# Kernel tuning notes

Measured on AMD Instinct MI355X. Metric: run time of the kernel, lower is better.

The kernel has to match this reference:

```python
import jax, jax.numpy as jnp
import numpy as np

G = 128          # number of point-cloud groups
DOWNSAMPLE = 256 # points per group
D = 256          # feature dim


def _pairwise_dist(x, y):
    # x: [G, n, d], y: [G, m, d] -> Euclidean distances [G, n, m]
    x2 = jnp.sum(x * x, axis=-1)[:, :, None]
    y2 = jnp.sum(y * y, axis=-1)[:, None, :]
    d2 = jnp.maximum(x2 + y2 - 2.0 * jnp.einsum('gnd,gmd->gnm', x, y), 0.0)
    # safe sqrt (zero diagonal has zero distance, avoid NaN grads)
    return jnp.where(d2 > 0, jnp.sqrt(jnp.where(d2 > 0, d2, 1.0)), 0.0)


def setup_inputs() -> dict:
    key = jax.random.key(0)
    k1, k2 = jax.random.split(key)
    inp = jax.random.normal(k1, (G * DOWNSAMPLE, D), dtype=jnp.float32)
    tgt = jax.random.normal(k2, (G * DOWNSAMPLE, D), dtype=jnp.float32)
    return {"input": inp, "target": tgt, "downsample": DOWNSAMPLE}


def reference(input, target, downsample):
    # MMDLoss.forward: reshape to (-1, downsample, D), batched energy distance, mean
    x = input.reshape(-1, downsample, input.shape[-1])   # [G, n, D]
    y = target.reshape(-1, downsample, target.shape[-1]) # [G, m, D]
    # Energy distance (geomloss 'energy' kernel k(x,y) = -||x-y||, uniform weights):
    # L = mean_ij ||x_i - y_j|| - 0.5 mean_ij ||x_i - x_j|| - 0.5 mean_ij ||y_i - y_j||
    d_xy = jnp.mean(_pairwise_dist(x, y), axis=(1, 2))  # [G]
    d_xx = jnp.mean(_pairwise_dist(x, x), axis=(1, 2))  # [G]
    d_yy = jnp.mean(_pairwise_dist(y, y), axis=(1, 2))  # [G]
    loss_per_group = d_xy - 0.5 * d_xx - 0.5 * d_yy
    return jnp.mean(loss_per_group)
```

## Files before the change

kernel.cpp:

```cpp
#include <hip/hip_runtime.h>
#include <hip/hip_bf16.h>
#include <stdint.h>
#include <string.h>

typedef __attribute__((ext_vector_type(8))) short short8;
typedef __attribute__((ext_vector_type(4))) float floatx4;
typedef unsigned short u16;

#define NPTS 256
#define DIM  256
#define TILE 128
#define BKN  64
#define NITN (DIM / BKN)

static __device__ __forceinline__ uint32_t cvtsq2(float a, float b, float& s) {
    __hip_bfloat162 h = __float22bfloat162_rn(float2{a, b});
    uint32_t d;
    memcpy(&d, &h, 4);
    const float lo = __builtin_bit_cast(float, d << 16);
    const float hi = __builtin_bit_cast(float, d & 0xFFFF0000u);
    s += lo * lo + hi * hi;
    return d;
}
static __device__ __forceinline__ uint4 cvt8(const float4 u, const float4 v, float& s) {
    uint4 r;
    r.x = cvtsq2(u.x, u.y, s); r.y = cvtsq2(u.z, u.w, s);
    r.z = cvtsq2(v.x, v.w == v.w ? v.w : v.w, s), r.z = cvtsq2(v.x, v.y, s); r.w = cvtsq2(v.z, v.w, s);
    return r;
}

__global__ __launch_bounds__(256)
void mmd_prep(const float* __restrict__ X, const float* __restrict__ Y,
              u16* __restrict__ Zb, float* __restrict__ nrm,
              int totalRows, int halfRows) {
    const int gid = blockIdx.x * 256 + threadIdx.x;
    const int row = gid >> 5;
    if (row >= totalRows) return;
    const int sub = gid & 31;
    const float* src = (row < halfRows ? X + (size_t)row * DIM
                                       : Y + (size_t)(row - halfRows) * DIM) + sub * 8;
    const float4 a = *(const float4*)src;
    const float4 b = *(const float4*)(src + 4);
    float s = 0.0f;
    uint4 p;
    p.x = cvtsq2(a.x, a.y, s); p.y = cvtsq2(a.z, a.w, s);
    p.z = cvtsq2(b.x, b.y, s); p.w = cvtsq2(b.z, b.w, s);
    *(uint4*)(Zb + (size_t)row * DIM + sub * 8) = p;
    s += __shfl_xor(s, 1); s += __shfl_xor(s, 2); s += __shfl_xor(s, 4);
    s += __shfl_xor(s, 8); s += __shfl_xor(s, 16);
    if (sub == 0) nrm[row] = s;
}

static __device__ __forceinline__ void stage_tile(
    const u16* __restrict__ Zrow0,
    u16* ldsbase,
    int k0, int wv, int lane) {
    #pragma unroll
    for (int j = 0; j < 4; ++j) {
        const int cid = (wv * 4 + j) * 64 + lane;
        const int row = cid >> 3;
        const int cs  = cid & 7;
        const int cg  = cs ^ (row & 7);
        const u16* src = Zrow0 + (size_t)row * DIM + k0 + cg * 8;
        u16* dst = ldsbase + (size_t)(wv * 4 + j) * 512;
        __builtin_amdgcn_global_load_lds(
            (const __attribute__((address_space(1))) uint32_t*)src,
            (__attribute__((address_space(3))) uint32_t*)dst, 16, 0, 0);
    }
}

__global__ __launch_bounds__(256, 2)
void mmd_main(const u16* __restrict__ Zb, const float* __restrict__ nrm,
              float* __restrict__ out, float scale, int G) {
    int g, t;
    const int f = blockIdx.x;
    if ((G & 7) == 0) { const int xcd = f & 7, j = f >> 3; g = (j / 10) * 8 + xcd; t = j % 10; }
    else              { g = f / 10; t = f % 10; }

    int ptype, ti, tj; float w;
    if (t < 4)      { ptype = 0; ti = t >> 1; tj = t & 1; w = 1.0f; }
    else if (t < 7) { int u = t - 4; ptype = 1; ti = (u == 2); tj = (u >= 1); w = (u == 1) ? -1.0f : -0.5f; }
    else            { int u = t - 7; ptype = 2; ti = (u == 2); tj = (u >= 1); w = (u == 1) ? -1.0f : -0.5f; }

    const int half = G * NPTS;
    const int pbase = (ptype == 2) ? half : 0;
    const int qbase = (ptype == 1) ? 0 : half;
    const size_t prow0 = (size_t)pbase + (size_t)g * NPTS + (size_t)ti * TILE;
    const size_t qrow0 = (size_t)qbase + (size_t)g * NPTS + (size_t)tj * TILE;
    const bool symdiag = (ptype != 0) && (ti == tj);

    const u16* ZP = Zb + prow0 * DIM;
    const u16* ZQ = Zb + qrow0 * DIM;

    __shared__ __align__(16) u16 As[2][TILE * BKN];
    __shared__ __align__(16) u16 Bs[2][TILE * BKN];
    __shared__ float rnormS[TILE];
    __shared__ float cnormS[TILE];
    __shared__ float wpart[4];

    const int tid  = threadIdx.x;
    const int lane = tid & 63;
    const int wv   = tid >> 6;
    const int quad = lane >> 4;
    const int l15  = lane & 15;
    const int wr   = (wv >> 1) * 64;
    const int wc   = (wv & 1) * 64;
    const int sw0  = (quad ^ (l15 & 7)) * 8;

    floatx4 acc[4][4];
    #pragma unroll
    for (int i = 0; i < 4; ++i)
        #pragma unroll
        for (int j = 0; j < 4; ++j) acc[i][j] = (floatx4)0.0f;

    if (tid < TILE) rnormS[tid] = nrm[prow0 + tid];
    else            cnormS[tid - TILE] = nrm[qrow0 + (tid - TILE)];

    stage_tile(ZP, As[0], 0, wv, lane);
    if (!symdiag) stage_tile(ZQ, Bs[0], 0, wv, lane);

    #pragma unroll
    for (int it = 0; it < NITN; ++it) {
        const int b = it & 1;
        __syncthreads();

        if (it + 1 < NITN) {
            stage_tile(ZP, As[b ^ 1], (it + 1) * BKN, wv, lane);
            if (!symdiag) stage_tile(ZQ, Bs[b ^ 1], (it + 1) * BKN, wv, lane);
        }

        const u16* abase = As[b];
        const u16* bbase = symdiag ? As[b] : Bs[b];
        #pragma unroll
        for (int ks = 0; ks < 2; ++ks) {
            const int kswz = ks * 32;
            short8 af[4], bfv[4];
            #pragma unroll
            for (int mi = 0; mi < 4; ++mi) {
                const int row = wr + mi * 16 + l15;
                af[mi] = *(const short8*)&abase[row * BKN + (sw0 ^ kswz)];
            }
            #pragma unroll
            for (int ni = 0; ni < 4; ++ni) {
                const int row = wc + ni * 16 + l15;
                bfv[ni] = *(const short8*)&bbase[row * BKN + (sw0 ^ kswz)];
            }
            #pragma unroll
            for (int mi = 0; mi < 4; ++mi)
                #pragma unroll
                for (int ni = 0; ni < 4; ++ni)
                    acc[mi][ni] = __builtin_amdgcn_mfma_f32_16x16x32_bf16(
                        af[mi], bfv[ni], acc[mi][ni], 0, 0, 0);
        }
    }

    float lsum = 0.0f;
    #pragma unroll
    for (int mi = 0; mi < 4; ++mi) {
        #pragma unroll
        for (int i = 0; i < 4; ++i) {
            const int r = wr + mi * 16 + quad * 4 + i;
            const float rv = rnormS[r];
            #pragma unroll
            for (int ni = 0; ni < 4; ++ni) {
                const int c = wc + ni * 16 + l15;
                float d2 = rv + cnormS[c] - 2.0f * acc[mi][ni][i];
                float s = sqrtf(fmaxf(d2, 0.0f));
                if (symdiag && (r == c)) s = 0.0f;
                lsum += s;
            }
        }
    }
    #pragma unroll
    for (int off = 32; off; off >>= 1) lsum += __shfl_down(lsum, off);
    if (lane == 0) wpart[wv] = lsum;
    __syncthreads();
    if (tid == 0) {
        float bs = wpart[0] + wpart[1] + wpart[2] + wpart[3];
        atomicAdd(out, bs * (w * scale));
    }
}

#define BK   32
#define NIT  (DIM / BK)
#define LDSS 40

__global__ __launch_bounds__(512, 4)
void mmd_pipe(const float* __restrict__ X, const float* __restrict__ Y,
              float* __restrict__ out, float scale, int G) {
    int g, t;
    const int f = blockIdx.x;
    if ((G & 7) == 0) { const int xcd = f & 7, j = f >> 3; g = (j / 10) * 8 + xcd; t = j % 10; }
    else              { g = f / 10; t = f % 10; }

    int ptype, ti, tj; float w;
    if (t < 4)      { ptype = 0; ti = t >> 1; tj = t & 1; w = 1.0f; }
    else if (t < 7) { int u = t - 4; ptype = 1; ti = (u == 2); tj = (u >= 1); w = (u == 1) ? -1.0f : -0.5f; }
    else            { int u = t - 7; ptype = 2; ti = (u == 2); tj = (u >= 1); w = (u == 1) ? -1.0f : -0.5f; }

    const float *Pf, *Qf;
    if (ptype == 0)      { Pf = X; Qf = Y; }
    else if (ptype == 1) { Pf = X; Qf = X; }
    else                 { Pf = Y; Qf = Y; }
    const bool symdiag = (ptype != 0) && (ti == tj);

    const size_t prow0 = (size_t)g * NPTS + (size_t)ti * TILE;
    const size_t qrow0 = (size_t)g * NPTS + (size_t)tj * TILE;

    __shared__ __align__(16) uint16_t As[2][TILE * LDSS];
    __shared__ __align__(16) uint16_t Bs[2][TILE * LDSS];
    __shared__ float rnorm[TILE];
    __shared__ float cnorm[TILE];
    __shared__ float wpart[8];

    const int tid  = threadIdx.x;
    const int lane = tid & 63;
    const int wv   = tid >> 6;
    const int quad = lane >> 4;
    const int l15  = lane & 15;
    const int rowbase = (wv & 3) * 32;
    const int colbase = (wv >> 2) * 64;

    const int prow = tid >> 2;
    const int pcol = (tid & 3) * 8;
    const float* gA = Pf + (prow0 + prow) * DIM + pcol;
    const float* gB = Qf + (qrow0 + prow) * DIM + pcol;
    const int woff = prow * LDSS + pcol;

    floatx4 acc[2][4];
    #pragma unroll
    for (int i = 0; i < 2; ++i)
        #pragma unroll
        for (int j = 0; j < 4; ++j) acc[i][j] = (floatx4)0.0f;

    float sqp = 0.0f, sqq = 0.0f;

    float4 ra0 = *(const float4*)(gA);
    float4 ra1 = *(const float4*)(gA + 4);
    float4 rb0 = *(const float4*)(gB);
    float4 rb1 = *(const float4*)(gB + 4);
    {
        uint4 pa, pb;
        pa.x = cvtsq2(ra0.x, ra0.y, sqp); pa.y = cvtsq2(ra0.z, ra0.w, sqp);
        pa.z = cvtsq2(ra1.x, ra1.y, sqp); pa.w = cvtsq2(ra1.z, ra1.w, sqp);
        pb.x = cvtsq2(rb0.x, rb0.y, sqq); pb.y = cvtsq2(rb0.z, rb0.w, sqq);
        pb.z = cvtsq2(rb1.x, rb1.y, sqq); pb.w = cvtsq2(rb1.z, rb1.w, sqq);
        *(uint4*)&As[0][woff] = pa;
        *(uint4*)&Bs[0][woff] = pb;
    }
    ra0 = *(const float4*)(gA + BK);
    ra1 = *(const float4*)(gA + BK + 4);
    rb0 = *(const float4*)(gB + BK);
    rb1 = *(const float4*)(gB + BK + 4);

    #pragma unroll
    for (int it = 0; it < NIT; ++it) {
        const int b = it & 1;
        __syncthreads();

        if (it < NIT - 1) {
            uint4 pa, pb;
            pa.x = cvtsq2(ra0.x, ra0.y, sqp); pa.y = cvtsq2(ra0.z, ra0.w, sqp);
            pa.z = cvtsq2(ra1.x, ra1.y, sqp); pa.w = cvtsq2(ra1.z, ra1.w, sqp);
            pb.x = cvtsq2(rb0.x, rb0.y, sqq); pb.y = cvtsq2(rb0.z, rb0.w, sqq);
            pb.z = cvtsq2(rb1.x, rb1.y, sqq); pb.w = cvtsq2(rb1.z, rb1.w, sqq);
            *(uint4*)&As[b ^ 1][woff] = pa;
            *(uint4*)&Bs[b ^ 1][woff] = pb;
        }
        if (it < NIT - 2) {
            const int k0 = (it + 2) * BK;
            ra0 = *(const float4*)(gA + k0);
            ra1 = *(const float4*)(gA + k0 + 4);
            rb0 = *(const float4*)(gB + k0);
            rb1 = *(const float4*)(gB + k0 + 4);
        }

        short8 af[2], bfr[4];
        #pragma unroll
        for (int mi = 0; mi < 2; ++mi)
            af[mi] = *(const short8*)&As[b][(rowbase + mi * 16 + l15) * LDSS + quad * 8];
        #pragma unroll
        for (int ni = 0; ni < 4; ++ni)
            bfr[ni] = *(const short8*)&Bs[b][(colbase + ni * 16 + l15) * LDSS + quad * 8];
        #pragma unroll
        for (int mi = 0; mi < 2; ++mi)
            #pragma unroll
            for (int ni = 0; ni < 4; ++ni)
                acc[mi][ni] = __builtin_amdgcn_mfma_f32_16x16x32_bf16(
                    af[mi], bfr[ni], acc[mi][ni], 0, 0, 0);
    }

    sqp += __shfl_xor(sqp, 1); sqp += __shfl_xor(sqp, 2);
    sqq += __shfl_xor(sqq, 1); sqq += __shfl_xor(sqq, 2);
    if ((tid & 3) == 0) { rnorm[prow] = sqp; cnorm[prow] = sqq; }
    __syncthreads();

    float lsum = 0.0f;
    #pragma unroll
    for (int mi = 0; mi < 2; ++mi) {
        #pragma unroll
        for (int i = 0; i < 4; ++i) {
            const int r = rowbase + mi * 16 + quad * 4 + i;
            const float rv = rnorm[r];
            #pragma unroll
            for (int ni = 0; ni < 4; ++ni) {
                const int c = colbase + ni * 16 + l15;
                float d2 = rv + cnorm[c] - 2.0f * acc[mi][ni][i];
                float s = sqrtf(fmaxf(d2, 0.0f));
                if (symdiag && (r == c)) s = 0.0f;
                lsum += s;
            }
        }
    }
    #pragma unroll
    for (int off = 32; off; off >>= 1) lsum += __shfl_down(lsum, off);
    if (lane == 0) wpart[wv] = lsum;
    __syncthreads();
    if (tid == 0) {
        float bs = 0.0f;
        #pragma unroll
        for (int i = 0; i < 8; ++i) bs += wpart[i];
        atomicAdd(out, bs * (w * scale));
    }
}

extern "C" void kernel_launch(void* const* d_in, const int* in_sizes, int n_in,
                              void* d_out, int out_size, void* d_ws, size_t ws_size,
                              hipStream_t stream) {
    const float* X = (const float*)d_in[0];
    const float* Y = (const float*)d_in[1];
    const int total_elems = in_sizes[0];
    const int G = total_elems / (NPTS * DIM);

    float* out = (float*)d_out;
    hipMemsetAsync(out, 0, sizeof(float) * out_size, stream);

    const float scale = 1.0f / ((float)NPTS * (float)NPTS * (float)G);

    const size_t rows = (size_t)2 * G * NPTS;
    const size_t zb_bytes  = rows * DIM * sizeof(u16);
    const size_t nrm_bytes = rows * sizeof(float);

    if (d_ws != nullptr && ws_size >= zb_bytes + nrm_bytes) {
        u16* Zb = (u16*)d_ws;
        float* nrm = (float*)((char*)d_ws + zb_bytes);
        const int pblocks = (int)(rows / 8);
        mmd_prep<<<pblocks, 256, 0, stream>>>(X, Y, Zb, nrm, (int)rows, G * NPTS);
        mmd_main<<<10 * G, 256, 0, stream>>>(Zb, nrm, out, scale, G);
    } else {
        mmd_pipe<<<10 * G, 512, 0, stream>>>(X, Y, out, scale, G);
    }
}
```

Measured before the change: 133.2 us.

## Use static device buffers and 512-thread blocks for bf16 MMD kernel

Result: faster. 124.2 us (-6.7%).

```diff
diff --git a/kernel.cpp b/kernel.cpp
--- a/kernel.cpp
+++ b/kernel.cpp
@@ -12,6 +12,10 @@
 #define TILE 128
 #define BKN  64
 #define NITN (DIM / BKN)
+#define GMAX 128
+
+__device__ __align__(16) static u16  g_Zb[(size_t)2 * GMAX * NPTS * DIM];
+__device__ static float              g_nrm[2 * GMAX * NPTS];
 
 static __device__ __forceinline__ uint32_t cvtsq2(float a, float b, float& s) {
     __hip_bfloat162 h = __float22bfloat162_rn(float2{a, b});
@@ -22,16 +26,9 @@
     s += lo * lo + hi * hi;
     return d;
 }
-static __device__ __forceinline__ uint4 cvt8(const float4 u, const float4 v, float& s) {
-    uint4 r;
-    r.x = cvtsq2(u.x, u.y, s); r.y = cvtsq2(u.z, u.w, s);
-    r.z = cvtsq2(v.x, v.w == v.w ? v.w : v.w, s), r.z = cvtsq2(v.x, v.y, s); r.w = cvtsq2(v.z, v.w, s);
-    return r;
-}
 
 __global__ __launch_bounds__(256)
 void mmd_prep(const float* __restrict__ X, const float* __restrict__ Y,
-              u16* __restrict__ Zb, float* __restrict__ nrm,
               int totalRows, int halfRows) {
     const int gid = blockIdx.x * 256 + threadIdx.x;
     const int row = gid >> 5;
@@ -45,10 +42,10 @@
     uint4 p;
     p.x = cvtsq2(a.x, a.y, s); p.y = cvtsq2(a.z, a.w, s);
     p.z = cvtsq2(b.x, b.y, s); p.w = cvtsq2(b.z, b.w, s);
-    *(uint4*)(Zb + (size_t)row * DIM + sub * 8) = p;
+    *(uint4*)(g_Zb + (size_t)row * DIM + sub * 8) = p;
     s += __shfl_xor(s, 1); s += __shfl_xor(s, 2); s += __shfl_xor(s, 4);
     s += __shfl_xor(s, 8); s += __shfl_xor(s, 16);
-    if (sub == 0) nrm[row] = s;
+    if (sub == 0) g_nrm[row] = s;
 }
 
 static __device__ __forceinline__ void stage_tile(
@@ -56,26 +53,24 @@
     u16* ldsbase,
     int k0, int wv, int lane) {
     #pragma unroll
-    for (int j = 0; j < 4; ++j) {
-        const int cid = (wv * 4 + j) * 64 + lane;
+    for (int j = 0; j < 2; ++j) {
+        const int cid = (wv * 2 + j) * 64 + lane;
         const int row = cid >> 3;
         const int cs  = cid & 7;
         const int cg  = cs ^ (row & 7);
         const u16* src = Zrow0 + (size_t)row * DIM + k0 + cg * 8;
-        u16* dst = ldsbase + (size_t)(wv * 4 + j) * 512;
+        u16* dst = ldsbase + (size_t)(wv * 2 + j) * 512;
         __builtin_amdgcn_global_load_lds(
             (const __attribute__((address_space(1))) uint32_t*)src,
             (__attribute__((address_space(3))) uint32_t*)dst, 16, 0, 0);
     }
 }
 
-__global__ __launch_bounds__(256, 2)
-void mmd_main(const u16* __restrict__ Zb, const float* __restrict__ nrm,
-              float* __restrict__ out, float scale, int G) {
+__global__ __launch_bounds__(512, 4)
+void mmd_main(float* __restrict__ out, float scale, int G) {
     int g, t;
     const int f = blockIdx.x;
-    if ((G & 7) == 0) { const int xcd = f & 7, j = f >> 3; g = (j / 10) * 8 + xcd; t = j % 10; }
-    else              { g = f / 10; t = f % 10; }
+    { const int xcd = f & 7, j = f >> 3; g = (j / 10) * 8 + xcd; t = j % 10; }
 
     int ptype, ti, tj; float w;
     if (t < 4)      { ptype = 0; ti = t >> 1; tj = t & 1; w = 1.0f; }
@@ -89,32 +84,32 @@
     const size_t qrow0 = (size_t)qbase + (size_t)g * NPTS + (size_t)tj * TILE;
     const bool symdiag = (ptype != 0) && (ti == tj);
 
-    const u16* ZP = Zb + prow0 * DIM;
-    const u16* ZQ = Zb + qrow0 * DIM;
+    const u16* ZP = g_Zb + prow0 * DIM;
+    const u16* ZQ = g_Zb + qrow0 * DIM;
 
     __shared__ __align__(16) u16 As[2][TILE * BKN];
     __shared__ __align__(16) u16 Bs[2][TILE * BKN];
     __shared__ float rnormS[TILE];
     __shared__ float cnormS[TILE];
-    __shared__ float wpart[4];
+    __shared__ float wpart[8];
 
     const int tid  = threadIdx.x;
     const int lane = tid & 63;
     const int wv   = tid >> 6;
     const int quad = lane >> 4;
     const int l15  = lane & 15;
-    const int wr   = (wv >> 1) * 64;
-    const int wc   = (wv & 1) * 64;
+    const int wr   = (wv & 3) * 32;
+    const int wc   = (wv >> 2) * 64;
     const int sw0  = (quad ^ (l15 & 7)) * 8;
 
-    floatx4 acc[4][4];
-    #pragma unroll
-    for (int i = 0; i < 4; ++i)
+    floatx4 acc[2][4];
+    #pragma unroll
+    for (int i = 0; i < 2; ++i)
         #pragma unroll
         for (int j = 0; j < 4; ++j) acc[i][j] = (floatx4)0.0f;
 
-    if (tid < TILE) rnormS[tid] = nrm[prow0 + tid];
-    else            cnormS[tid - TILE] = nrm[qrow0 + (tid - TILE)];
+    if (tid < TILE)            rnormS[tid] = g_nrm[prow0 + tid];
+    else if (tid < 2 * TILE)   cnormS[tid - TILE] = g_nrm[qrow0 + (tid - TILE)];
 
     stage_tile(ZP, As[0], 0, wv, lane);
     if (!symdiag) stage_tile(ZQ, Bs[0], 0, wv, lane);
@@ -134,9 +129,9 @@
         #pragma unroll
         for (int ks = 0; ks < 2; ++ks) {
             const int kswz = ks * 32;
-            short8 af[4], bfv[4];
-            #pragma unroll
-            for (int mi = 0; mi < 4; ++mi) {
+            short8 af[2], bfv[4];
+            #pragma unroll
+            for (int mi = 0; mi < 2; ++mi) {
                 const int row = wr + mi * 16 + l15;
                 af[mi] = *(const short8*)&abase[row * BKN + (sw0 ^ kswz)];
             }
@@ -146,7 +141,7 @@
                 bfv[ni] = *(const short8*)&bbase[row * BKN + (sw0 ^ kswz)];
             }
             #pragma unroll
-            for (int mi = 0; mi < 4; ++mi)
+            for (int mi = 0; mi < 2; ++mi)
                 #pragma unroll
                 for (int ni = 0; ni < 4; ++ni)
                     acc[mi][ni] = __builtin_amdgcn_mfma_f32_16x16x32_bf16(
@@ -156,7 +151,7 @@
 
     float lsum = 0.0f;
     #pragma unroll
-    for (int mi = 0; mi < 4; ++mi) {
+    for (int mi = 0; mi < 2; ++mi) {
         #pragma unroll
         for (int i = 0; i < 4; ++i) {
             const int r = wr + mi * 16 + quad * 4 + i;
@@ -176,7 +171,9 @@
     if (lane == 0) wpart[wv] = lsum;
     __syncthreads();
     if (tid == 0) {
-        float bs = wpart[0] + wpart[1] + wpart[2] + wpart[3];
+        float bs = 0.0f;
+        #pragma unroll
+        for (int i = 0; i < 8; ++i) bs += wpart[i];
         atomicAdd(out, bs * (w * scale));
     }
 }
@@ -337,16 +334,11 @@
 
     const float scale = 1.0f / ((float)NPTS * (float)NPTS * (float)G);
 
-    const size_t rows = (size_t)2 * G * NPTS;
-    const size_t zb_bytes  = rows * DIM * sizeof(u16);
-    const size_t nrm_bytes = rows * sizeof(float);
-
-    if (d_ws != nullptr && ws_size >= zb_bytes + nrm_bytes) {
-        u16* Zb = (u16*)d_ws;
-        float* nrm = (float*)((char*)d_ws + zb_bytes);
-        const int pblocks = (int)(rows / 8);
-        mmd_prep<<<pblocks, 256, 0, stream>>>(X, Y, Zb, nrm, (int)rows, G * NPTS);
-        mmd_main<<<10 * G, 256, 0, stream>>>(Zb, nrm, out, scale, G);
+    if (G <= GMAX && (G & 7) == 0) {
+        const int rows = 2 * G * NPTS;
+        const int pblocks = rows / 8;
+        mmd_prep<<<pblocks, 256, 0, stream>>>(X, Y, rows, G * NPTS);
+        mmd_main<<<10 * G, 512, 0, stream>>>(out, scale, G);
     } else {
         mmd_pipe<<<10 * G, 512, 0, stream>>>(X, Y, out, scale, G);
     }
```
